# Kernel optimization log

Hardware: AMD Instinct MI355X
Metric: run time of the kernel (lower is better)

Reference implementation:

```python
import jax, jax.numpy as jnp
import numpy as np

N = 100000   # nodes
E = 3200000  # edges (avg degree 32)
F_IN = 128   # node feature dim (lazy in_channels)
C = 16       # GAT out_channels, heads=1
ED = 2       # edge_dim
B = 512      # graphs in batch
OUT_X = 64; OUT_Y = 64; ROT = 4
EPS = 1e-5


def _bn(x, g, b):
    # BatchNorm1d in training mode: biased batch variance, eps=1e-5
    mu = x.mean(0, keepdims=True)
    var = x.var(0, keepdims=True)
    return g * (x - mu) * jax.lax.rsqrt(var + EPS) + b


def _gat(x, src, dst, edge_attr, W, We, att_s, att_d, att_e, bias):
    # PyG GATConv, heads=1: self-loops added with fill_value='mean' edge attrs
    n = x.shape[0]
    deg = jax.ops.segment_sum(jnp.ones_like(dst, jnp.float32), dst, num_segments=n)
    loop_attr = jax.ops.segment_sum(edge_attr, dst, num_segments=n) / jnp.maximum(deg, 1.0)[:, None]
    idx = jnp.arange(n)
    src_f = jnp.concatenate([src, idx])
    dst_f = jnp.concatenate([dst, idx])
    ea = jnp.concatenate([edge_attr, loop_attr], axis=0)  # [E+N, ED]
    h = x @ W                      # [N, C]
    a_s = h @ att_s                # [N]
    a_d = h @ att_d                # [N]
    a_e = (ea @ We) @ att_e        # [E+N]
    logits = jax.nn.leaky_relu(a_s[src_f] + a_d[dst_f] + a_e, 0.2)
    m = jax.ops.segment_max(logits, dst_f, num_segments=n)  # every node has a self-loop
    ex = jnp.exp(logits - m[dst_f])
    alpha = ex / jax.ops.segment_sum(ex, dst_f, num_segments=n)[dst_f]
    return jax.ops.segment_sum(alpha[:, None] * h[src_f], dst_f, num_segments=n) + bias


def _glorot(k, shp):
    lim = float(np.sqrt(6.0 / (shp[0] + shp[1])))
    return jax.random.uniform(k, shp, jnp.float32, -lim, lim)


def setup_inputs() -> dict:
    key = jax.random.key(0)
    k = jax.random.split(key, 48)
    d = {}
    d['x'] = jax.random.normal(k[0], (N, F_IN), jnp.float32)
    d['edge_index'] = jax.random.randint(k[1], (2, E), 0, N)
    d['edge_attr'] = jax.random.normal(k[2], (E, ED), jnp.float32)
    d['batch'] = jnp.sort(jax.random.randint(k[3], (N,), 0, B))
    # gat1
    d['W1'] = _glorot(k[4], (F_IN, C)); d['We1'] = _glorot(k[5], (ED, C))
    d['as1'] = 0.1 * jax.random.normal(k[6], (C,)); d['ad1'] = 0.1 * jax.random.normal(k[7], (C,))
    d['ae1'] = 0.1 * jax.random.normal(k[8], (C,)); d['b1'] = jnp.zeros((C,), jnp.float32)
    # norm1 (BatchNorm on nodes)
    d['g1'] = 1.0 + 0.1 * jax.random.normal(k[9], (C,)); d['bb1'] = 0.1 * jax.random.normal(k[10], (C,))
    # gat2
    d['W2'] = _glorot(k[11], (C, C)); d['We2'] = _glorot(k[12], (ED, C))
    d['as2'] = 0.1 * jax.random.normal(k[13], (C,)); d['ad2'] = 0.1 * jax.random.normal(k[14], (C,))
    d['ae2'] = 0.1 * jax.random.normal(k[15], (C,)); d['b2'] = jnp.zeros((C,), jnp.float32)
    # D2RL MLP tail
    d['gL1'] = 1.0 + 0.1 * jax.random.normal(k[16], (C,)); d['bL1'] = 0.1 * jax.random.normal(k[17], (C,))
    d['Wl1'] = _glorot(k[18], (C, C)); d['bl1'] = 0.1 * jax.random.normal(k[19], (C,))
    d['gL2'] = 1.0 + 0.1 * jax.random.normal(k[20], (2 * C,)); d['bL2'] = 0.1 * jax.random.normal(k[21], (2 * C,))
    d['Wl2'] = _glorot(k[22], (2 * C, C)); d['bl2'] = 0.1 * jax.random.normal(k[23], (C,))
    d['gL3'] = 1.0 + 0.1 * jax.random.normal(k[24], (2 * C,)); d['bL3'] = 0.1 * jax.random.normal(k[25], (2 * C,))
    d['Wl3'] = _glorot(k[26], (2 * C, C)); d['bl3'] = 0.1 * jax.random.normal(k[27], (C,))
    d['Wx'] = _glorot(k[28], (C, OUT_X)); d['bx'] = 0.1 * jax.random.normal(k[29], (OUT_X,))
    d['Wy'] = _glorot(k[30], (C, OUT_Y)); d['by'] = 0.1 * jax.random.normal(k[31], (OUT_Y,))
    d['Wr'] = _glorot(k[32], (C, ROT)); d['br'] = 0.1 * jax.random.normal(k[33], (ROT,))
    return d


def reference(x, edge_index, edge_attr, batch,
              W1, We1, as1, ad1, ae1, b1, g1, bb1,
              W2, We2, as2, ad2, ae2, b2,
              gL1, bL1, Wl1, bl1, gL2, bL2, Wl2, bl2, gL3, bL3, Wl3, bl3,
              Wx, bx, Wy, by, Wr, br):
    src, dst = edge_index[0], edge_index[1]
    h = jax.nn.relu(_gat(x, src, dst, edge_attr, W1, We1, as1, ad1, ae1, b1))
    h = _bn(h, g1, bb1)
    h = jax.nn.relu(_gat(h, src, dst, edge_attr, W2, We2, as2, ad2, ae2, b2))
    # MeanAggregation over graphs
    cnt = jax.ops.segment_sum(jnp.ones((h.shape[0],), jnp.float32), batch, num_segments=B)
    xe = jax.ops.segment_sum(h, batch, num_segments=B) / jnp.maximum(cnt, 1.0)[:, None]  # [B, C]
    z = _bn(xe, gL1, bL1)
    z = jax.nn.relu(z @ Wl1 + bl1)
    z = _bn(jnp.concatenate([z, xe], axis=1), gL2, bL2)
    z = jax.nn.relu(z @ Wl2 + bl2)
    z = _bn(jnp.concatenate([z, xe], axis=1), gL3, bL3)
    z = jax.nn.relu(z @ Wl3 + bl3)
    xx = jax.nn.softmax(z @ Wx + bx, axis=1)
    y = jax.nn.softmax(z @ Wy + by, axis=1)
    rot = jax.nn.softmax(z @ Wr + br, axis=1)
    return (xx, y, rot)
```

## Files before the change

### kernel.cpp

```cpp
#include <hip/hip_runtime.h>
#include <hip/hip_fp16.h>
#include <math.h>

#define C 16
#define FIN 128

typedef unsigned int u32x2 __attribute__((ext_vector_type(2)));
typedef float f32x4 __attribute__((ext_vector_type(4)));

__global__ __launch_bounds__(256) void k_gemm1(
    const float* __restrict__ x, const float* __restrict__ W,
    const float* __restrict__ asw, const float* __restrict__ adw,
    __half* __restrict__ hh, float* __restrict__ a_s, float* __restrict__ a_d, int n) {
  __shared__ float xs[64 * 129];
  __shared__ float Ws[FIN * C];
  __shared__ float pAs[4][64], pAd[4][64];
  int t = threadIdx.x;
  int node0 = blockIdx.x * 64;
  for (int i = t; i < FIN * C; i += 256) Ws[i] = W[i];
  for (int i = t; i < 64 * FIN; i += 256) {
    int r = i >> 7, c = i & 127;
    int node = node0 + r;
    xs[r * 129 + c] = (node < n) ? x[(size_t)node * FIN + c] : 0.f;
  }
  __syncthreads();
  int nn = t & 63, cg = (t >> 6) * 4, grp = t >> 6;
  float a0 = 0.f, a1 = 0.f, a2 = 0.f, a3 = 0.f;
  const float* xr = &xs[nn * 129];
  #pragma unroll 8
  for (int k = 0; k < FIN; ++k) {
    float xv = xr[k];
    const float* wr = &Ws[k * C + cg];
    a0 += xv * wr[0]; a1 += xv * wr[1]; a2 += xv * wr[2]; a3 += xv * wr[3];
  }
  int node = node0 + nn;
  if (node < n) {
    __half2 p0 = __floats2half2_rn(a0, a1), p1 = __floats2half2_rn(a2, a3);
    unsigned u0, u1;
    memcpy(&u0, &p0, 4); memcpy(&u1, &p1, 4);
    *(uint2*)(hh + (size_t)node * 16 + cg) = make_uint2(u0, u1);
  }
  pAs[grp][nn] = a0 * asw[cg] + a1 * asw[cg + 1] + a2 * asw[cg + 2] + a3 * asw[cg + 3];
  pAd[grp][nn] = a0 * adw[cg] + a1 * adw[cg + 1] + a2 * adw[cg + 2] + a3 * adw[cg + 3];
  __syncthreads();
  if (t < 64 && node0 + t < n) {
    a_s[node0 + t] = pAs[0][t] + pAs[1][t] + pAs[2][t] + pAs[3][t];
    a_d[node0 + t] = pAd[0][t] + pAd[1][t] + pAd[2][t] + pAd[3][t];
  }
}

__global__ __launch_bounds__(512) void k_scan1(const int* __restrict__ counts,
                                               int* __restrict__ bsum, int n) {
  __shared__ int sd[512];
  int i = blockIdx.x * 512 + threadIdx.x;
  sd[threadIdx.x] = (i < n) ? counts[i] : 0;
  __syncthreads();
  for (int s = 256; s > 0; s >>= 1) {
    if (threadIdx.x < s) sd[threadIdx.x] += sd[threadIdx.x + s];
    __syncthreads();
  }
  if (threadIdx.x == 0) bsum[blockIdx.x] = sd[0];
}

__global__ __launch_bounds__(512) void k_scan2(int* __restrict__ bsum,
                                               int* __restrict__ offs,
                                               int nblk, int n) {
  __shared__ int sd[512];
  int t = threadIdx.x;
  int v = (t < nblk) ? bsum[t] : 0;
  sd[t] = v;
  __syncthreads();
  for (int off = 1; off < 512; off <<= 1) {
    int x = (t >= off) ? sd[t - off] : 0;
    __syncthreads();
    sd[t] += x;
    __syncthreads();
  }
  if (t < nblk) bsum[t] = sd[t] - v;
  if (t == nblk - 1) offs[n] = sd[t];
}

__global__ __launch_bounds__(512) void k_scan3(const int* __restrict__ counts,
                                               const int* __restrict__ bsum,
                                               int* __restrict__ offs, int n) {
  __shared__ int sd[512];
  int t = threadIdx.x;
  int i = blockIdx.x * 512 + t;
  int v = (i < n) ? counts[i] : 0;
  sd[t] = v;
  __syncthreads();
  for (int off = 1; off < 512; off <<= 1) {
    int x = (t >= off) ? sd[t - off] : 0;
    __syncthreads();
    sd[t] += x;
    __syncthreads();
  }
  if (i < n) offs[i] = bsum[blockIdx.x] + sd[t] - v;
}

__global__ __launch_bounds__(256) void k_p1count(
    const int* __restrict__ dst, int* __restrict__ histT,
    int ne, int chunk, int G, int nbin) {
  __shared__ int hist[512];
  int g = blockIdx.x, t = threadIdx.x;
  for (int i = t; i < nbin; i += 256) hist[i] = 0;
  __syncthreads();
  int e0 = g * chunk, e1 = e0 + chunk; if (e1 > ne) e1 = ne;
  for (int e = e0 + t; e < e1; e += 256) atomicAdd(&hist[dst[e] >> 8], 1);
  __syncthreads();
  for (int i = t; i < nbin; i += 256) histT[i * G + g] = hist[i];
}

__global__ __launch_bounds__(256) void k_p1scat(
    const int* __restrict__ src, const int* __restrict__ dst,
    const float* __restrict__ ea, const int* __restrict__ histS,
    const float* __restrict__ We1, const float* __restrict__ ae1,
    const float* __restrict__ We2, const float* __restrict__ ae2,
    uint2* __restrict__ tmpR, int ne, int chunk, int G, int nbin) {
  __shared__ int cur[512];
  int g = blockIdx.x, t = threadIdx.x;
  for (int i = t; i < nbin; i += 256) cur[i] = histS[i * G + g];
  float w01 = 0.f, w11 = 0.f, w02 = 0.f, w12 = 0.f;
  #pragma unroll
  for (int c = 0; c < C; ++c) {
    w01 += We1[c] * ae1[c]; w11 += We1[C + c] * ae1[c];
    w02 += We2[c] * ae2[c]; w12 += We2[C + c] * ae2[c];
  }
  __syncthreads();
  int e0 = g * chunk, e1 = e0 + chunk; if (e1 > ne) e1 = ne;
  for (int e = e0 + t; e < e1; e += 256) {
    int d = dst[e];
    int pos = atomicAdd(&cur[d >> 8], 1);
    u32x2 ab = __builtin_nontemporal_load((const u32x2*)(ea + 2 * (size_t)e));
    float ax = __uint_as_float(ab.x);
    float ay = __uint_as_float(ab.y);
    __half2 hp = __floats2half2_rn(ax * w01 + ay * w11, ax * w02 + ay * w12);
    unsigned hb;
    memcpy(&hb, &hp, 4);
    tmpR[pos] = make_uint2((unsigned)src[e] | ((unsigned)(d & 255) << 24), hb);
  }
}

__global__ __launch_bounds__(256) void k_p2(
    const uint2* __restrict__ tmpR, const int* __restrict__ histS,
    uint2* __restrict__ bucket, int* __restrict__ offs,
    int G, int nbin, int n, int ne) {
  __shared__ int hist[256], scn[256], cur[256];
  int b = blockIdx.x, t = threadIdx.x;
  int cs0 = histS[b * G];
  int cs1 = (b + 1 < nbin) ? histS[(b + 1) * G] : ne;
  hist[t] = 0;
  __syncthreads();
  for (int i = cs0 + t; i < cs1; i += 256) {
    u32x2 r = __builtin_nontemporal_load((const u32x2*)(tmpR + i));
    atomicAdd(&hist[r.x >> 24], 1);
  }
  __syncthreads();
  int v = hist[t];
  scn[t] = v;
  __syncthreads();
  for (int off = 1; off < 256; off <<= 1) {
    int x = (t >= off) ? scn[t - off] : 0;
    __syncthreads();
    scn[t] += x;
    __syncthreads();
  }
  int excl = scn[t] - v;
  int node = b * 256 + t;
  if (node <= n) offs[node] = cs0 + excl;
  if (b == 0 && t == 0) offs[n] = ne;
  cur[t] = cs0 + excl;
  __syncthreads();
  for (int i = cs0 + t; i < cs1; i += 256) {
    u32x2 r = __builtin_nontemporal_load((const u32x2*)(tmpR + i));
    int pos = atomicAdd(&cur[r.x >> 24], 1);
    bucket[pos] = make_uint2(r.x & 0x00FFFFFFu, r.y);
  }
}

__global__ __launch_bounds__(256) void k_hist_rank(
    const int* __restrict__ dst, int* __restrict__ counts,
    int* __restrict__ rank, int ne) {
  int e = blockIdx.x * 256 + threadIdx.x;
  if (e < ne) rank[e] = atomicAdd(&counts[dst[e]], 1);
}

__global__ __launch_bounds__(256) void k_scatter(
    const int* __restrict__ src, const int* __restrict__ dst,
    const float2* __restrict__ ea, const int* __restrict__ offs,
    const int* __restrict__ rank,
    const float* __restrict__ We1, const float* __restrict__ ae1,
    const float* __restrict__ We2, const float* __restrict__ ae2,
    uint2* __restrict__ bucket, int ne) {
  int e = blockIdx.x * 256 + threadIdx.x;
  if (e >= ne) return;
  float w01 = 0.f, w11 = 0.f, w02 = 0.f, w12 = 0.f;
  #pragma unroll
  for (int c = 0; c < C; ++c) {
    w01 += We1[c] * ae1[c]; w11 += We1[C + c] * ae1[c];
    w02 += We2[c] * ae2[c]; w12 += We2[C + c] * ae2[c];
  }
  int d = dst[e];
  float2 a = ea[e];
  __half2 hp = __floats2half2_rn(a.x * w01 + a.y * w11, a.x * w02 + a.y * w12);
  unsigned hb;
  memcpy(&hb, &hp, 4);
  bucket[offs[d] + rank[e]] = make_uint2((unsigned)src[e], hb);
}

__global__ __launch_bounds__(256) void k_gather(
    const uint2* __restrict__ bucket, const int* __restrict__ offs,
    const float* __restrict__ a_s, const float* __restrict__ a_d,
    const __half* __restrict__ hh, const float* __restrict__ bias,
    float* __restrict__ outv, float* __restrict__ bnsum, float* __restrict__ bnsq,
    int lay, int do_bn, int n) {
  __shared__ float sbn[32];
  int t = threadIdx.x;
  if (do_bn) {
    if (t < 32) sbn[t] = 0.f;
    __syncthreads();
  }

  int node = blockIdx.x * 64 + (t >> 2);
  int l = t & 3, f = l & 1, p = l >> 1;

  float acc[8];
  #pragma unroll
  for (int j = 0; j < 8; ++j) acc[j] = 0.f;
  float den = 0.f, ssum = 0.f;
  int o0 = 0, o1 = 0;
  float adi = 0.f, asi = 0.f;
  if (node < n) {
    o0 = offs[node]; o1 = offs[node + 1];
    adi = a_d[node]; asi = a_s[node];
    int e = o0 + p;
    u32x2 r = {0u, 0u};
    if (e < o1) r = __builtin_nontemporal_load((const u32x2*)(bucket + e));
    while (e < o1) {
      int en = e + 2;
      u32x2 rn = {0u, 0u};
      if (en < o1) rn = __builtin_nontemporal_load((const u32x2*)(bucket + en));
      int s = (int)r.x;
      unsigned scb = r.y;
      __half2 sc2;
      memcpy(&sc2, &scb, 4);
      float se = lay ? __high2float(sc2) : __low2float(sc2);
      float asv = a_s[s];
      uint4 hv = *(const uint4*)(hh + ((size_t)s << 4) + (f << 3));
      float lg = asv + adi + se;
      lg = lg > 0.f ? lg : 0.2f * lg;
      float ex = __expf(lg);
      den += ex; ssum += se;
      __half2 t0, t1, t2, t3;
      memcpy(&t0, &hv.x, 4); memcpy(&t1, &hv.y, 4);
      memcpy(&t2, &hv.z, 4); memcpy(&t3, &hv.w, 4);
      float2 g0 = __half22float2(t0), g1 = __half22float2(t1);
      float2 g2 = __half22float2(t2), g3 = __half22float2(t3);
      acc[0] += ex * g0.x; acc[1] += ex * g0.y;
      acc[2] += ex * g1.x; acc[3] += ex * g1.y;
      acc[4] += ex * g2.x; acc[5] += ex * g2.y;
      acc[6] += ex * g3.x; acc[7] += ex * g3.y;
      r = rn; e = en;
    }
  }
  den += __shfl_xor(den, 2);
  ssum += __shfl_xor(ssum, 2);
  #pragma unroll
  for (int j = 0; j < 8; ++j) acc[j] += __shfl_xor(acc[j], 2);

  float v[8];
  #pragma unroll
  for (int j = 0; j < 8; ++j) v[j] = 0.f;
  if (node < n) {
    float dgc = fmaxf((float)(o1 - o0), 1.f);
    float lg = asi + adi + ssum / dgc;
    lg = lg > 0.f ? lg : 0.2f * lg;
    float exs = __expf(lg);
    uint4 hv = *(const uint4*)(hh + ((size_t)node << 4) + (f << 3));
    __half2 t0, t1, t2, t3;
    memcpy(&t0, &hv.x, 4); memcpy(&t1, &hv.y, 4);
    memcpy(&t2, &hv.z, 4); memcpy(&t3, &hv.w, 4);
    float2 g0 = __half22float2(t0), g1 = __half22float2(t1);
    float2 g2 = __half22float2(t2), g3 = __half22float2(t3);
    float hs[8] = {g0.x, g0.y, g1.x, g1.y, g2.x, g2.y, g3.x, g3.y};
    float inv = 1.f / (den + exs);
    const float* bp = bias + f * 8;
    #pragma unroll
    for (int j = 0; j < 8; ++j)
      v[j] = fmaxf((acc[j] + exs * hs[j]) * inv + bp[j], 0.f);
    if (p == 0) {
      f32x4 w0 = {v[0], v[1], v[2], v[3]};
      f32x4 w1 = {v[4], v[5], v[6], v[7]};
      float* op = outv + ((size_t)node << 4) + f * 8;
      __builtin_nontemporal_store(w0, (f32x4*)op);
      __builtin_nontemporal_store(w1, (f32x4*)(op + 4));
    }
  }

  if (do_bn) {
    float sv[8], qv[8];
    bool act = (node < n) && (p == 0);
    #pragma unroll
    for (int j = 0; j < 8; ++j) {
      sv[j] = act ? v[j] : 0.f;
      qv[j] = sv[j] * sv[j];
    }
    #pragma unroll
    for (int j = 0; j < 8; ++j) {
      sv[j] += __shfl_down(sv[j], 4);  qv[j] += __shfl_down(qv[j], 4);
      sv[j] += __shfl_down(sv[j], 8);  qv[j] += __shfl_down(qv[j], 8);
      sv[j] += __shfl_down(sv[j], 16); qv[j] += __shfl_down(qv[j], 16);
      sv[j] += __shfl_down(sv[j], 32); qv[j] += __shfl_down(qv[j], 32);
    }
    if ((t & 63) < 2) {
      #pragma unroll
      for (int j = 0; j < 8; ++j) {
        atomicAdd(&sbn[f * 8 + j], sv[j]);
        atomicAdd(&sbn[16 + f * 8 + j], qv[j]);
      }
    }
    __syncthreads();
    if (t < 16) atomicAdd(&bnsum[t], sbn[t]);
    else if (t < 32) atomicAdd(&bnsq[t - 16], sbn[t]);
  }
}

__global__ void k_bnp(const float* __restrict__ bnsum, const float* __restrict__ bnsq,
                      const float* __restrict__ g, const float* __restrict__ bb,
                      float* __restrict__ scale, float* __restrict__ shift, float invn) {
  int c = threadIdx.x;
  if (c >= C) return;
  float mean = bnsum[c] * invn;
  float var = bnsq[c] * invn - mean * mean;
  float s = g[c] * rsqrtf(var + 1e-5f);
  scale[c] = s; shift[c] = bb[c] - mean * s;
}

__global__ __launch_bounds__(256) void k_node2(
    const float* __restrict__ outv, const float* __restrict__ scale,
    const float* __restrict__ shift, const float* __restrict__ W2,
    const float* __restrict__ asw, const float* __restrict__ adw,
    __half* __restrict__ hh, float* __restrict__ a_s, float* __restrict__ a_d, int n) {
  __shared__ float w2s[C * C];
  if (threadIdx.x < C * C) w2s[threadIdx.x] = W2[threadIdx.x];
  __syncthreads();
  int i = blockIdx.x * 256 + threadIdx.x;
  if (i >= n) return;
  float hn[C];
  #pragma unroll
  for (int c = 0; c < C; ++c) hn[c] = outv[(size_t)i * C + c] * scale[c] + shift[c];
  float h2[C];
  #pragma unroll
  for (int j = 0; j < C; ++j) {
    float acc = 0.f;
    #pragma unroll
    for (int c = 0; c < C; ++c) acc += hn[c] * w2s[c * C + j];
    h2[j] = acc;
  }
  float hs = 0.f, hd = 0.f;
  #pragma unroll
  for (int j = 0; j < C; ++j) { hs += h2[j] * asw[j]; hd += h2[j] * adw[j]; }
  a_s[i] = hs; a_d[i] = hd;
  unsigned wbits[8];
  #pragma unroll
  for (int j = 0; j < 8; ++j) {
    __half2 hq = __floats2half2_rn(h2[2 * j], h2[2 * j + 1]);
    memcpy(&wbits[j], &hq, 4);
  }
  uint4* hp = (uint4*)(hh + (size_t)i * 16);
  hp[0] = make_uint4(wbits[0], wbits[1], wbits[2], wbits[3]);
  hp[1] = make_uint4(wbits[4], wbits[5], wbits[6], wbits[7]);
}

__global__ void k_gstart(const int* __restrict__ batch, int* __restrict__ gs,
                         int n, int B_) {
  int g = blockIdx.x * blockDim.x + threadIdx.x;
  if (g > B_) return;
  if (g == B_) { gs[B_] = n; return; }
  int lo = 0, hi = n;
  while (lo < hi) { int mid = (lo + hi) >> 1; if (batch[mid] < g) lo = mid + 1; else hi = mid; }
  gs[g] = lo;
}

__global__ __launch_bounds__(256) void k_xe(
    const float* __restrict__ outv, const int* __restrict__ gs,
    float* __restrict__ xe, int B_) {
  int wave = blockIdx.x * 4 + (threadIdx.x >> 6);
  if (wave >= B_) return;
  int lane = threadIdx.x & 63;
  int c = lane & 15, sub = lane >> 4;
  int base = gs[wave], end = gs[wave + 1];
  float s = 0.f;
  for (int n0 = base + sub; n0 < end; n0 += 4) s += outv[(size_t)n0 * C + c];
  s += __shfl_down(s, 32);
  s += __shfl_down(s, 16);
  if (lane < 16) xe[(size_t)wave * C + c] = s / fmaxf((float)(end - base), 1.f);
}

__global__ __launch_bounds__(512) void k_tail_z3(
    const float* __restrict__ xe_in,
    const float* __restrict__ gL1, const float* __restrict__ bL1,
    const float* __restrict__ Wl1, const float* __restrict__ bl1,
    const float* __restrict__ gL2, const float* __restrict__ bL2,
    const float* __restrict__ Wl2, const float* __restrict__ bl2,
    const float* __restrict__ gL3, const float* __restrict__ bL3,
    const float* __restrict__ Wl3, const float* __restrict__ bl3,
    float* __restrict__ z3buf, int B_) {
  __shared__ float ssum[2 * C], ssq[2 * C], sc[2 * C], sh[2 * C];
  int t = threadIdx.x;
  float invB = 1.f / (float)B_;
  float xe[C];
  #pragma unroll
  for (int c = 0; c < C; ++c) xe[c] = xe_in[(size_t)t * C + c];

  if (t < 2 * C) { ssum[t] = 0.f; ssq[t] = 0.f; }
  __syncthreads();
  #pragma unroll
  for (int c = 0; c < C; ++c) {
    float s = xe[c], q = xe[c] * xe[c];
    for (int o = 32; o > 0; o >>= 1) { s += __shfl_down(s, o); q += __shfl_down(q, o); }
    if ((t & 63) == 0) { atomicAdd(&ssum[c], s); atomicAdd(&ssq[c], q); }
  }
  __syncthreads();
  if (t < C) {
    float mean = ssum[t] * invB, var = ssq[t] * invB - mean * mean;
    float s = gL1[t] * rsqrtf(var + 1e-5f);
    sc[t] = s; sh[t] = bL1[t] - mean * s;
  }
  __syncthreads();
  float z[C];
  #pragma unroll
  for (int j = 0; j < C; ++j) {
    float acc = bl1[j];
    #pragma unroll
    for (int c = 0; c < C; ++c) acc += (xe[c] * sc[c] + sh[c]) * Wl1[c * C + j];
    z[j] = fmaxf(acc, 0.f);
  }
  __syncthreads();

  if (t < 2 * C) { ssum[t] = 0.f; ssq[t] = 0.f; }
  __syncthreads();
  #pragma unroll
  for (int c = 0; c < C; ++c) {
    float s = z[c], q = z[c] * z[c];
    for (int o = 32; o > 0; o >>= 1) { s += __shfl_down(s, o); q += __shfl_down(q, o); }
    if ((t & 63) == 0) { atomicAdd(&ssum[c], s); atomicAdd(&ssq[c], q); }
    float s2 = xe[c], q2 = xe[c] * xe[c];
    for (int o = 32; o > 0; o >>= 1) { s2 += __shfl_down(s2, o); q2 += __shfl_down(q2, o); }
    if ((t & 63) == 0) { atomicAdd(&ssum[C + c], s2); atomicAdd(&ssq[C + c], q2); }
  }
  __syncthreads();
  if (t < 2 * C) {
    float mean = ssum[t] * invB, var = ssq[t] * invB - mean * mean;
    float s = gL2[t] * rsqrtf(var + 1e-5f);
    sc[t] = s; sh[t] = bL2[t] - mean * s;
  }
  __syncthreads();
  float z2[C];
  #pragma unroll
  for (int j = 0; j < C; ++j) {
    float acc = bl2[j];
    #pragma unroll
    for (int c = 0; c < C; ++c) acc += (z[c] * sc[c] + sh[c]) * Wl2[c * C + j];
    #pragma unroll
    for (int c = 0; c < C; ++c) acc += (xe[c] * sc[C + c] + sh[C + c]) * Wl2[(C + c) * C + j];
    z2[j] = fmaxf(acc, 0.f);
  }
  __syncthreads();

  if (t < 2 * C) { ssum[t] = 0.f; ssq[t] = 0.f; }
  __syncthreads();
  #pragma unroll
  for (int c = 0; c < C; ++c) {
    float s = z2[c], q = z2[c] * z2[c];
    for (int o = 32; o > 0; o >>= 1) { s += __shfl_down(s, o); q += __shfl_down(q, o); }
    if ((t & 63) == 0) { atomicAdd(&ssum[c], s); atomicAdd(&ssq[c], q); }
    float s2 = xe[c], q2 = xe[c] * xe[c];
    for (int o = 32; o > 0; o >>= 1) { s2 += __shfl_down(s2, o); q2 += __shfl_down(q2, o); }
    if ((t & 63) == 0) { atomicAdd(&ssum[C + c], s2); atomicAdd(&ssq[C + c], q2); }
  }
  __syncthreads();
  if (t < 2 * C) {
    float mean = ssum[t] * invB, var = ssq[t] * invB - mean * mean;
    float s = gL3[t] * rsqrtf(var + 1e-5f);
    sc[t] = s; sh[t] = bL3[t] - mean * s;
  }
  __syncthreads();
  #pragma unroll
  for (int j = 0; j < C; ++j) {
    float acc = bl3[j];
    #pragma unroll
    for (int c = 0; c < C; ++c) acc += (z2[c] * sc[c] + sh[c]) * Wl3[c * C + j];
    #pragma unroll
    for (int c = 0; c < C; ++c) acc += (xe[c] * sc[C + c] + sh[C + c]) * Wl3[(C + c) * C + j];
    z3buf[(size_t)t * C + j] = fmaxf(acc, 0.f);
  }
}

__global__ __launch_bounds__(256) void k_heads(
    const float* __restrict__ z3buf,
    const float* __restrict__ Wx, const float* __restrict__ bx,
    const float* __restrict__ Wy, const float* __restrict__ by,
    const float* __restrict__ Wr, const float* __restrict__ br,
    float* __restrict__ out, int B_) {
  int wv = blockIdx.x * 4 + (threadIdx.x >> 6);
  if (wv >= B_) return;
  int lane = threadIdx.x & 63;
  float z[C];
  #pragma unroll
  for (int c = 0; c < C; ++c) z[c] = z3buf[(size_t)wv * C + c];

  float ax = bx[lane];
  #pragma unroll
  for (int c = 0; c < C; ++c) ax += z[c] * Wx[c * 64 + lane];
  float m = ax;
  #pragma unroll
  for (int o = 32; o > 0; o >>= 1) m = fmaxf(m, __shfl_xor(m, o));
  float e = __expf(ax - m);
  float s = e;
  #pragma unroll
  for (int o = 32; o > 0; o >>= 1) s += __shfl_xor(s, o);
  out[(size_t)wv * 64 + lane] = e / s;

  float ay = by[lane];
  #pragma unroll
  for (int c = 0; c < C; ++c) ay += z[c] * Wy[c * 64 + lane];
  m = ay;
  #pragma unroll
  for (int o = 32; o > 0; o >>= 1) m = fmaxf(m, __shfl_xor(m, o));
  e = __expf(ay - m);
  s = e;
  #pragma unroll
  for (int o = 32; o > 0; o >>= 1) s += __shfl_xor(s, o);
  out[(size_t)B_ * 64 + (size_t)wv * 64 + lane] = e / s;

  if (lane < 4) {
    float ar = br[lane];
    #pragma unroll
    for (int c = 0; c < C; ++c) ar += z[c] * Wr[c * 4 + lane];
    float mr = ar;
    mr = fmaxf(mr, __shfl_xor(mr, 1));
    mr = fmaxf(mr, __shfl_xor(mr, 2));
    float er = __expf(ar - mr);
    float sr = er;
    sr += __shfl_xor(sr, 1);
    sr += __shfl_xor(sr, 2);
    out[(size_t)B_ * 128 + (size_t)wv * 4 + lane] = er / sr;
  }
}

extern "C" void kernel_launch(void* const* d_in, const int* in_sizes, int n_in,
                              void* d_out, int out_size, void* d_ws, size_t ws_size,
                              hipStream_t stream) {
  const float* x     = (const float*)d_in[0];
  const int*   eidx  = (const int*)d_in[1];
  const float* eattr = (const float*)d_in[2];
  const int*   batch = (const int*)d_in[3];
  const float* W1  = (const float*)d_in[4];
  const float* We1 = (const float*)d_in[5];
  const float* as1 = (const float*)d_in[6];
  const float* ad1 = (const float*)d_in[7];
  const float* ae1 = (const float*)d_in[8];
  const float* b1  = (const float*)d_in[9];
  const float* g1  = (const float*)d_in[10];
  const float* bb1 = (const float*)d_in[11];
  const float* W2  = (const float*)d_in[12];
  const float* We2 = (const float*)d_in[13];
  const float* as2 = (const float*)d_in[14];
  const float* ad2 = (const float*)d_in[15];
  const float* ae2 = (const float*)d_in[16];
  const float* b2  = (const float*)d_in[17];
  const float* gL1 = (const float*)d_in[18];
  const float* bL1 = (const float*)d_in[19];
  const float* Wl1 = (const float*)d_in[20];
  const float* bl1 = (const float*)d_in[21];
  const float* gL2 = (const float*)d_in[22];
  const float* bL2 = (const float*)d_in[23];
  const float* Wl2 = (const float*)d_in[24];
  const float* bl2 = (const float*)d_in[25];
  const float* gL3 = (const float*)d_in[26];
  const float* bL3 = (const float*)d_in[27];
  const float* Wl3 = (const float*)d_in[28];
  const float* bl3 = (const float*)d_in[29];
  const float* Wx  = (const float*)d_in[30];
  const float* bx  = (const float*)d_in[31];
  const float* Wy  = (const float*)d_in[32];
  const float* by  = (const float*)d_in[33];
  const float* Wr  = (const float*)d_in[34];
  const float* br  = (const float*)d_in[35];

  int N = in_sizes[3];
  int E = in_sizes[2] / 2;
  int B = out_size / 132;

  const int* src = eidx;
  const int* dst = eidx + E;

  const int G = 128;
  int nbin = (N + 255) >> 8;
  int nscan = nbin * G;
  int chunk = (E + G - 1) / G;
  int nblk2 = (nscan + 511) / 512;

  char* w = (char*)d_ws;
  size_t o = 0;
  auto alloc = [&](size_t bytes) { char* p = w + o; o += (bytes + 15) & ~15ull; return p; };
  uint2*  bucket = (uint2*)alloc((size_t)E * 8);
  uint2*  tmpR   = (uint2*)alloc((size_t)E * 8);
  __half* hh     = (__half*)alloc((size_t)N * C * 2);
  float*  outv   = (float*)alloc((size_t)N * C * 4);
  float*  a_s    = (float*)alloc((size_t)N * 4);
  float*  a_d    = (float*)alloc((size_t)N * 4);
  int*    counts = (int*)alloc((size_t)(N + 4) * 4);
  int*    offs   = (int*)alloc((size_t)(N + 4) * 4);
  int*    histT  = (int*)alloc((size_t)(nscan + 4) * 4);
  int*    histS  = (int*)alloc((size_t)(nscan + 4) * 4);
  int*    bsum   = (int*)alloc((size_t)(nblk2 + 516) * 4);
  float*  bn     = (float*)alloc(64 * 4);
  float*  xe     = (float*)alloc((size_t)B * C * 4);
  int*    gs     = (int*)alloc((size_t)(B + 4) * 4);
  float*  z3buf  = (float*)alloc((size_t)B * C * 4);
  size_t need = o;

  bool radix = (need <= ws_size) && (nbin <= 512) && (nblk2 <= 512) && (N <= (1 << 24));

  hipMemsetAsync(bn, 0, 32 * 4, stream);
  k_gemm1<<<(N + 63) / 64, 256, 0, stream>>>(x, W1, as1, ad1, hh, a_s, a_d, N);

  if (radix) {
    k_p1count<<<G, 256, 0, stream>>>(dst, histT, E, chunk, G, nbin);
    k_scan1<<<nblk2, 512, 0, stream>>>(histT, bsum, nscan);
    k_scan2<<<1, 512, 0, stream>>>(bsum, histS, nblk2, nscan);
    k_scan3<<<nblk2, 512, 0, stream>>>(histT, bsum, histS, nscan);
    k_p1scat<<<G, 256, 0, stream>>>(src, dst, eattr, histS,
                                    We1, ae1, We2, ae2, tmpR, E, chunk, G, nbin);
    k_p2<<<nbin, 256, 0, stream>>>(tmpR, histS, bucket, offs, G, nbin, N, E);
  } else {
    int* rank = (int*)tmpR;
    int nblk = (N + 511) / 512;
    int ebl = (E + 255) / 256;
    hipMemsetAsync(counts, 0, (size_t)N * 4, stream);
    k_hist_rank<<<ebl, 256, 0, stream>>>(dst, counts, rank, E);
    k_scan1<<<nblk, 512, 0, stream>>>(counts, bsum, N);
    k_scan2<<<1, 512, 0, stream>>>(bsum, offs, nblk, N);
    k_scan3<<<nblk, 512, 0, stream>>>(counts, bsum, offs, N);
    k_scatter<<<ebl, 256, 0, stream>>>(src, dst, (const float2*)eattr, offs, rank,
                                       We1, ae1, We2, ae2, bucket, E);
  }

  int nbl = (N + 255) / 256;
  k_gather<<<(N + 63) / 64, 256, 0, stream>>>(bucket, offs, a_s, a_d, hh, b1,
                                              outv, bn, bn + 16, 0, 1, N);
  k_bnp<<<1, 64, 0, stream>>>(bn, bn + 16, g1, bb1, bn + 32, bn + 48, 1.f / (float)N);
  k_node2<<<nbl, 256, 0, stream>>>(outv, bn + 32, bn + 48, W2, as2, ad2, hh, a_s, a_d, N);
  k_gather<<<(N + 63) / 64, 256, 0, stream>>>(bucket, offs, a_s, a_d, hh, b2,
                                              outv, bn, bn + 16, 1, 0, N);
  k_gstart<<<(B + 1 + 255) / 256, 256, 0, stream>>>(batch, gs, N, B);
  k_xe<<<(B + 3) / 4, 256, 0, stream>>>(outv, gs, xe, B);
  k_tail_z3<<<1, B, 0, stream>>>(xe, gL1, bL1, Wl1, bl1, gL2, bL2, Wl2, bl2,
                                 gL3, bL3, Wl3, bl3, z3buf, B);
  k_heads<<<(B + 3) / 4, 256, 0, stream>>>(z3buf, Wx, bx, Wy, by, Wr, br,
                                           (float*)d_out, B);
}
```

Baseline: 698.8 us.

## Fuse first-layer GAT gather into radix bucket pass k_p2

Extends the second radix pass so that, after placing edges into per-node buckets, each thread immediately computes the layer-1 GAT softmax aggregation for its own node. It also emits the BN partial sums, and it replaces the separate k_gather launch on the radix path. The goal is to save a kernel launch and reuse the block's freshly written bucket data while it is likely cache-resident. The cost is that one thread serially walks each node's edge list (about 32 on average), with 16 register accumulators. That gives much less memory-level parallelism and coalescing than the old gather kernel, which used 4 threads per node.

```diff
diff --git a/kernel.cpp b/kernel.cpp
--- a/kernel.cpp
+++ b/kernel.cpp
@@ -141,23 +141,28 @@
   }
 }
 
-__global__ __launch_bounds__(256) void k_p2(
+__global__ __launch_bounds__(256) void k_p2g(
     const uint2* __restrict__ tmpR, const int* __restrict__ histS,
     uint2* __restrict__ bucket, int* __restrict__ offs,
+    const float* __restrict__ a_s, const float* __restrict__ a_d,
+    const __half* __restrict__ hh, const float* __restrict__ bias,
+    float* __restrict__ outv, float* __restrict__ bnsum, float* __restrict__ bnsq,
     int G, int nbin, int n, int ne) {
   __shared__ int hist[256], scn[256], cur[256];
+  __shared__ float sbn[32];
   int b = blockIdx.x, t = threadIdx.x;
   int cs0 = histS[b * G];
   int cs1 = (b + 1 < nbin) ? histS[(b + 1) * G] : ne;
   hist[t] = 0;
+  if (t < 32) sbn[t] = 0.f;
   __syncthreads();
   for (int i = cs0 + t; i < cs1; i += 256) {
     u32x2 r = __builtin_nontemporal_load((const u32x2*)(tmpR + i));
     atomicAdd(&hist[r.x >> 24], 1);
   }
   __syncthreads();
-  int v = hist[t];
-  scn[t] = v;
+  int cnt = hist[t];
+  scn[t] = cnt;
   __syncthreads();
   for (int off = 1; off < 256; off <<= 1) {
     int x = (t >= off) ? scn[t - off] : 0;
@@ -165,7 +170,7 @@
     scn[t] += x;
     __syncthreads();
   }
-  int excl = scn[t] - v;
+  int excl = scn[t] - cnt;
   int node = b * 256 + t;
   if (node <= n) offs[node] = cs0 + excl;
   if (b == 0 && t == 0) offs[n] = ne;
@@ -176,6 +181,88 @@
     int pos = atomicAdd(&cur[r.x >> 24], 1);
     bucket[pos] = make_uint2(r.x & 0x00FFFFFFu, r.y);
   }
+  __threadfence();
+  __syncthreads();
+
+  float vout[C];
+  #pragma unroll
+  for (int j = 0; j < C; ++j) vout[j] = 0.f;
+  if (node < n) {
+    int o0 = cs0 + excl, o1 = o0 + cnt;
+    float adi = a_d[node], asi = a_s[node];
+    float acc[C];
+    #pragma unroll
+    for (int j = 0; j < C; ++j) acc[j] = 0.f;
+    float den = 0.f, ssum = 0.f;
+    for (int e = o0; e < o1; ++e) {
+      uint2 rec = bucket[e];
+      int s = (int)rec.x;
+      unsigned scb = rec.y;
+      __half2 sc2;
+      memcpy(&sc2, &scb, 4);
+      float se = __low2float(sc2);
+      float asv = a_s[s];
+      const uint4* hp = (const uint4*)(hh + ((size_t)s << 4));
+      uint4 h0 = hp[0], h1 = hp[1];
+      float lg = asv + adi + se;
+      lg = lg > 0.f ? lg : 0.2f * lg;
+      float ex = __expf(lg);
+      den += ex; ssum += se;
+      __half2 q0, q1, q2, q3, q4, q5, q6, q7;
+      memcpy(&q0, &h0.x, 4); memcpy(&q1, &h0.y, 4);
+      memcpy(&q2, &h0.z, 4); memcpy(&q3, &h0.w, 4);
+      memcpy(&q4, &h1.x, 4); memcpy(&q5, &h1.y, 4);
+      memcpy(&q6, &h1.z, 4); memcpy(&q7, &h1.w, 4);
+      float2 g0 = __half22float2(q0), g1 = __half22float2(q1);
+      float2 g2 = __half22float2(q2), g3 = __half22float2(q3);
+      float2 g4 = __half22float2(q4), g5 = __half22float2(q5);
+      float2 g6 = __half22float2(q6), g7 = __half22float2(q7);
+      acc[0] += ex * g0.x;  acc[1] += ex * g0.y;
+      acc[2] += ex * g1.x;  acc[3] += ex * g1.y;
+      acc[4] += ex * g2.x;  acc[5] += ex * g2.y;
+      acc[6] += ex * g3.x;  acc[7] += ex * g3.y;
+      acc[8] += ex * g4.x;  acc[9] += ex * g4.y;
+      acc[10] += ex * g5.x; acc[11] += ex * g5.y;
+      acc[12] += ex * g6.x; acc[13] += ex * g6.y;
+      acc[14] += ex * g7.x; acc[15] += ex * g7.y;
+    }
+    float dgc = fmaxf((float)cnt, 1.f);
+    float lg = asi + adi + ssum / dgc;
+    lg = lg > 0.f ? lg : 0.2f * lg;
+    float exs = __expf(lg);
+    const uint4* hp = (const uint4*)(hh + ((size_t)node << 4));
+    uint4 h0 = hp[0], h1 = hp[1];
+    __half2 q0, q1, q2, q3, q4, q5, q6, q7;
+    memcpy(&q0, &h0.x, 4); memcpy(&q1, &h0.y, 4);
+    memcpy(&q2, &h0.z, 4); memcpy(&q3, &h0.w, 4);
+    memcpy(&q4, &h1.x, 4); memcpy(&q5, &h1.y, 4);
+    memcpy(&q6, &h1.z, 4); memcpy(&q7, &h1.w, 4);
+    float hs[C] = {
+      __low2float(q0), __high2float(q0), __low2float(q1), __high2float(q1),
+      __low2float(q2), __high2float(q2), __low2float(q3), __high2float(q3),
+      __low2float(q4), __high2float(q4), __low2float(q5), __high2float(q5),
+      __low2float(q6), __high2float(q6), __low2float(q7), __high2float(q7)};
+    float inv = 1.f / (den + exs);
+    #pragma unroll
+    for (int j = 0; j < C; ++j)
+      vout[j] = fmaxf((acc[j] + exs * hs[j]) * inv + bias[j], 0.f);
+    float* op = outv + ((size_t)node << 4);
+    #pragma unroll
+    for (int j = 0; j < 4; ++j) {
+      f32x4 wv = {vout[4 * j], vout[4 * j + 1], vout[4 * j + 2], vout[4 * j + 3]};
+      __builtin_nontemporal_store(wv, (f32x4*)(op + 4 * j));
+    }
+  }
+
+  #pragma unroll
+  for (int j = 0; j < C; ++j) {
+    float s = vout[j], q = vout[j] * vout[j];
+    for (int o = 32; o > 0; o >>= 1) { s += __shfl_down(s, o); q += __shfl_down(q, o); }
+    if ((t & 63) == 0) { atomicAdd(&sbn[j], s); atomicAdd(&sbn[16 + j], q); }
+  }
+  __syncthreads();
+  if (t < 16) atomicAdd(&bnsum[t], sbn[t]);
+  else if (t < 32) atomicAdd(&bnsq[t - 16], sbn[t]);
 }
 
 __global__ __launch_bounds__(256) void k_hist_rank(
@@ -634,7 +721,9 @@
     k_scan3<<<nblk2, 512, 0, stream>>>(histT, bsum, histS, nscan);
     k_p1scat<<<G, 256, 0, stream>>>(src, dst, eattr, histS,
                                     We1, ae1, We2, ae2, tmpR, E, chunk, G, nbin);
-    k_p2<<<nbin, 256, 0, stream>>>(tmpR, histS, bucket, offs, G, nbin, N, E);
+    k_p2g<<<nbin, 256, 0, stream>>>(tmpR, histS, bucket, offs,
+                                    a_s, a_d, hh, b1, outv, bn, bn + 16,
+                                    G, nbin, N, E);
   } else {
     int* rank = (int*)tmpR;
     int nblk = (N + 511) / 512;
@@ -646,11 +735,11 @@
     k_scan3<<<nblk, 512, 0, stream>>>(counts, bsum, offs, N);
     k_scatter<<<ebl, 256, 0, stream>>>(src, dst, (const float2*)eattr, offs, rank,
                                        We1, ae1, We2, ae2, bucket, E);
+    k_gather<<<(N + 63) / 64, 256, 0, stream>>>(bucket, offs, a_s, a_d, hh, b1,
+                                                outv, bn, bn + 16, 0, 1, N);
   }
 
   int nbl = (N + 255) / 256;
-  k_gather<<<(N + 63) / 64, 256, 0, stream>>>(bucket, offs, a_s, a_d, hh, b1,
-                                              outv, bn, bn + 16, 0, 1, N);
   k_bnp<<<1, 64, 0, stream>>>(bn, bn + 16, g1, bb1, bn + 32, bn + 48, 1.f / (float)N);
   k_node2<<<nbl, 256, 0, stream>>>(outv, bn + 32, bn + 48, W2, as2, ad2, hh, a_s, a_d, N);
   k_gather<<<(N + 63) / 64, 256, 0, stream>>>(bucket, offs, a_s, a_d, hh, b2,
```

New measurement: 740.0 us. 5.9% more time.
